# Kernel optimization log

Measured on AMD Instinct MI355X. Metric: run time of the kernel, lower is better.

The kernel has to match this reference:

```python
import jax, jax.numpy as jnp
import numpy as np

B, N, OBS, HID, H = 8, 1024, 64, 192, 3
D = HID // H  # head_dim = 64
ALPHA = 0.2   # LeakyReLU negative slope
NEG = -9e15   # mask value from torch code (-9000000000000000.0)


def gat_layer(h, adj, W, a):
    """Multi-head GAT layer, math-identical to the torch per-head loop.
    h: (B,N,F_in), adj: (N,N), W: (H,F_in,D), a: (H,2D).
    Concat-score a^T [Wh_i || Wh_j] is split into a_l^T Wh_i + a_r^T Wh_j
    (broadcast-add) to avoid materializing the N^2 x 2D tensor.
    """
    Wh = jnp.einsum('bni,hid->bhnd', h, W)           # (B,H,N,D)
    d = Wh.shape[-1]
    s_i = jnp.einsum('bhnd,hd->bhn', Wh, a[:, :d])   # a_l . Wh_i
    s_j = jnp.einsum('bhnd,hd->bhn', Wh, a[:, d:])   # a_r . Wh_j
    e = s_i[..., :, None] + s_j[..., None, :]        # (B,H,N,N)
    e = jnp.where(e > 0, e, ALPHA * e)               # LeakyReLU
    e = jnp.where(adj > 0, e, NEG)                   # adjacency mask
    attn = jax.nn.softmax(e, axis=-1)                # (dropout=0 in eval)
    out = jnp.einsum('bhnm,bhmd->bhnd', attn, Wh)    # weighted aggregate
    b, nh, n, _ = out.shape
    return out.transpose(0, 2, 1, 3).reshape(b, n, nh * d)  # concat heads


def setup_inputs() -> dict:
    key = jax.random.key(0)
    k1, k2, k3, k4, k5 = jax.random.split(key, 5)
    h = jax.random.normal(k1, (B, N, OBS), dtype=jnp.float32)
    adj = jnp.ones((N, N), dtype=jnp.float32)  # graph_type='full'
    # xavier_uniform-style scale (gain=1.414)
    def xav(k, shape, fan_in, fan_out):
        lim = 1.414 * np.sqrt(6.0 / (fan_in + fan_out))
        return jax.random.uniform(k, shape, jnp.float32, -lim, lim)
    W1 = xav(k2, (H, OBS, D), OBS, D)
    a1 = xav(k3, (H, 2 * D), 2 * D, 1)
    W2 = xav(k4, (H, HID, D), HID, D)
    a2 = xav(k5, (H, 2 * D), 2 * D, 1)
    return {"h": h, "adj": adj, "W1": W1, "a1": a1, "W2": W2, "a2": a2}


def reference(h, adj, W1, a1, W2, a2):
    x = gat_layer(h, adj, W1, a1)   # (B,N,HID)
    x = jax.nn.elu(x)               # inter-layer nonlinearity
    x = gat_layer(x, adj, W2, a2)   # (B,N,HID)
    return x
```

## Files before the change

kernel.cpp:

```cpp
#include <hip/hip_runtime.h>
#include <math.h>

#define Bc   8
#define Nc   1024
#define OBSc 64
#define HIDc 192
#define NHc  3
#define Dc   64
#define ALPHAc 0.2f

typedef __attribute__((ext_vector_type(8))) _Float16 half8;
typedef __attribute__((ext_vector_type(4))) float floatx4;


__global__ __launch_bounds__(256) void k_proj1(
    const float* __restrict__ xin, const float* __restrict__ W1,
    const float* __restrict__ a1, _Float16* __restrict__ WhT,
    float* __restrict__ si, float* __restrict__ sj, float* __restrict__ Mp1,
    const float* __restrict__ adj, unsigned long long* __restrict__ adjb,
    const float* __restrict__ W2, _Float16* __restrict__ W2T)
{
    const int tid = threadIdx.x;
    const int bh  = blockIdx.y;

    if (bh == Bc * NHc) {
        const int px = blockIdx.x, wv = tid >> 6, lane = tid & 63;
        for (int r8 = 0; r8 < 8; ++r8) {
            const int i = px * 32 + wv * 8 + r8;
            unsigned long long word = 0;
            for (int g = 0; g < 16; ++g) {
                bool c = adj[(size_t)i * Nc + g * 64 + lane] > 0.f;
                unsigned long long bal = __ballot(c);
                if (lane == g) word = bal;
            }
            if (lane < 16) adjb[(size_t)i * 16 + lane] = word;
        }
        if (px < 12) {
            for (int e = px * 3072 + tid; e < px * 3072 + 3072; e += 256) {
                int t = e & 7, ln = (e >> 3) & 63, p = (e >> 9) & 1, nh = (e >> 10) & 1;
                int g = e >> 11; int ks = g % 6, hh = g / 6;
                int k = ks * 32 + (ln >> 4) * 8 + t;
                int d = nh * 32 + p * 16 + (ln & 15);
                W2T[e] = (_Float16)W2[((size_t)hh * HIDc + k) * Dc + d];
            }
        }
        return;
    }

    __shared__ union {
        _Float16 Bs[64][OBSc + 8];
        _Float16 Ts[64][40];
    } u;
    __shared__ float spsAi[32], spsAj[32], spsBi[32], spsBj[32];

    const int b = bh / NHc, hh = bh % NHc;
    const int row0 = blockIdx.x * 32;

    for (int e = tid; e < OBSc * 64; e += 256) {
        int k = e >> 6, d = e & 63;
        u.Bs[d][k] = (_Float16)W1[(size_t)hh * OBSc * 64 + e];
    }
    __syncthreads();

    const int lane = tid & 63, wv = tid >> 6;
    const int mblk = (wv & 1) * 16, nhalf = (wv >> 1) * 32;
    const int fr = lane & 15, fq = lane >> 4;
    floatx4 acc0 = {0.f,0.f,0.f,0.f}, acc1 = {0.f,0.f,0.f,0.f};
    const int row = row0 + mblk + fr;

#pragma unroll
    for (int ks = 0; ks < OBSc / 32; ++ks) {
        const int k0 = ks * 32 + fq * 8;
        const float* xr = xin + ((size_t)b * Nc + row) * OBSc + k0;
        float4 u0 = *(const float4*)xr;
        float4 u1 = *(const float4*)(xr + 4);
        half8 af;
        af[0] = (_Float16)u0.x; af[1] = (_Float16)u0.y;
        af[2] = (_Float16)u0.z; af[3] = (_Float16)u0.w;
        af[4] = (_Float16)u1.x; af[5] = (_Float16)u1.y;
        af[6] = (_Float16)u1.z; af[7] = (_Float16)u1.w;
        half8 b0 = *(const half8*)&u.Bs[nhalf + fr][k0];
        half8 b1 = *(const half8*)&u.Bs[nhalf + 16 + fr][k0];
        acc0 = __builtin_amdgcn_mfma_f32_16x16x32_f16(af, b0, acc0, 0, 0, 0);
        acc1 = __builtin_amdgcn_mfma_f32_16x16x32_f16(af, b1, acc1, 0, 0, 0);
    }

    const float al0 = a1[hh * 2 * Dc + nhalf + fr];
    const float al1 = a1[hh * 2 * Dc + nhalf + 16 + fr];
    const float ar0 = a1[hh * 2 * Dc + Dc + nhalf + fr];
    const float ar1 = a1[hh * 2 * Dc + Dc + nhalf + 16 + fr];
    float pi[4], pj[4];
#pragma unroll
    for (int r = 0; r < 4; ++r) {
        pi[r] = acc0[r] * al0 + acc1[r] * al1;
        pj[r] = acc0[r] * ar0 + acc1[r] * ar1;
        for (int off = 8; off >= 1; off >>= 1) {
            pi[r] += __shfl_xor(pi[r], off, 64);
            pj[r] += __shfl_xor(pj[r], off, 64);
        }
    }
    if (fr == 0) {
#pragma unroll
        for (int r = 0; r < 4; ++r) {
            int lr = mblk + fq * 4 + r;
            if (nhalf == 0) { spsAi[lr] = pi[r]; spsAj[lr] = pj[r]; }
            else            { spsBi[lr] = pi[r]; spsBj[lr] = pj[r]; }
        }
    }
    __syncthreads();
    if (tid < 64) {
        float vj = -INFINITY;
        if (tid < 32) {
            size_t g = (size_t)bh * Nc + row0 + tid;
            si[g] = spsAi[tid] + spsBi[tid];
            vj    = spsAj[tid] + spsBj[tid];
            sj[g] = vj;
        }
        float mv = vj;
        for (int off = 32; off >= 1; off >>= 1) mv = fmaxf(mv, __shfl_xor(mv, off, 64));
        if (tid == 0) Mp1[bh * 32 + blockIdx.x] = mv;
    }

#pragma unroll
    for (int nt = 0; nt < 2; ++nt) {
        const int d = nhalf + nt * 16 + fr;
        floatx4 acc = nt ? acc1 : acc0;
#pragma unroll
        for (int p = 0; p < 2; ++p) {
            union { unsigned int w; _Float16 h[2]; } pk;
            pk.h[0] = (_Float16)acc[2 * p];
            pk.h[1] = (_Float16)acc[2 * p + 1];
            *(unsigned int*)&u.Ts[d][mblk + fq * 4 + 2 * p] = pk.w;
        }
    }
    __syncthreads();
    {
        const int c2 = tid >> 6, lane2 = tid & 63;
        const int fr2 = lane2 & 15, fq2 = lane2 >> 4;
        const int jt = row0 >> 5;
        uint4 v = *(const uint4*)&u.Ts[c2 * 16 + fr2][fq2 * 8];
        *(uint4*)&WhT[(size_t)(bh * 32 + jt) * 2048 + tid * 8] = v;
    }
}

__global__ __launch_bounds__(384, 2) void k_fused(
    const _Float16* __restrict__ WhT1,
    const float* __restrict__ si1, const float* __restrict__ sj1,
    const float* __restrict__ Mp1, const unsigned long long* __restrict__ adjb,
    const _Float16* __restrict__ W2T, const float* __restrict__ a2,
    _Float16* __restrict__ WhT2,
    float* __restrict__ si2, float* __restrict__ sj2, float* __restrict__ Mp2)
{
    __shared__ union {
        struct { float red[6][64][20]; float zs[6][16]; } ag;
        _Float16 Ts3[3][64][24];
    } uR;
    __shared__ _Float16 xhs[16][208];
    __shared__ float sp2i[6][16], sp2j[6][16];

    const int tid = threadIdx.x, wv = tid >> 6, lane = tid & 63;
    const int b = blockIdx.x >> 6, c16 = blockIdx.x & 63;
    const int row0 = c16 * 16;
    const int hh = wv >> 1, kh = wv & 1;
    const int bh = b * NHc + hh;
    const int fr = lane & 15, fq = lane >> 4;
    const int row = row0 + fr;

    float mpv = Mp1[bh * 32 + (lane & 31)];
    for (int off = 16; off >= 1; off >>= 1) mpv = fmaxf(mpv, __shfl_xor(mpv, off, 64));
    const float s_i = si1[(size_t)bh * Nc + row];
    const float em  = s_i + mpv;
    const float m_i = fmaxf(em, ALPHAc * em);

    const float* sjr = sj1 + (size_t)bh * Nc;
    const unsigned long long* arow = adjb + (size_t)row * 16;
    const _Float16* Bp = WhT1 + (size_t)bh * 65536 + (size_t)kh * 32768 + lane * 8;

    floatx4 acc[4] = {{0.f,0.f,0.f,0.f},{0.f,0.f,0.f,0.f},
                      {0.f,0.f,0.f,0.f},{0.f,0.f,0.f,0.f}};
    float zacc = 0.f;

    float4 sa = *(const float4*)&sjr[(kh * 16) * 32 + fq * 8];
    float4 sb = *(const float4*)&sjr[(kh * 16) * 32 + fq * 8 + 4];
    unsigned long long w = arow[(kh * 16) >> 1];
    half8 bfr0 = *(const half8*)(Bp);
    half8 bfr1 = *(const half8*)(Bp + 512);
    half8 bfr2 = *(const half8*)(Bp + 1024);
    half8 bfr3 = *(const half8*)(Bp + 1536);

#pragma unroll
    for (int s16 = 0; s16 < 16; ++s16) {
        const int s = kh * 16 + s16;
        float4 nsa, nsb; unsigned long long nw;
        half8 nb0, nb1, nb2, nb3;
        if (s16 < 15) {
            const int jn = (s + 1) * 32 + fq * 8;
            nsa = *(const float4*)&sjr[jn];
            nsb = *(const float4*)&sjr[jn + 4];
            nw  = arow[(s + 1) >> 1];
            const _Float16* bn = Bp + (size_t)(s16 + 1) * 2048;
            nb0 = *(const half8*)(bn);
            nb1 = *(const half8*)(bn + 512);
            nb2 = *(const half8*)(bn + 1024);
            nb3 = *(const half8*)(bn + 1536);
        }
        const int bb = (s & 1) * 32 + fq * 8;
        const float sv[8] = {sa.x, sa.y, sa.z, sa.w, sb.x, sb.y, sb.z, sb.w};
        float p[8];
        if (w == ~0ULL) {
#pragma unroll
            for (int t = 0; t < 8; ++t) {
                float e = s_i + sv[t];
                e = fmaxf(e, ALPHAc * e) - m_i;
                p[t] = __expf(e);
            }
        } else {
#pragma unroll
            for (int t = 0; t < 8; ++t) {
                float e = s_i + sv[t];
                e = fmaxf(e, ALPHAc * e) - m_i;
                e = ((w >> (bb + t)) & 1) ? e : -1e30f;
                p[t] = __expf(e);
            }
        }
        zacc += ((p[0] + p[1]) + (p[2] + p[3])) + ((p[4] + p[5]) + (p[6] + p[7]));
        union { half8 v; _Float16 h[8]; } A;
#pragma unroll
        for (int t = 0; t < 8; ++t) A.h[t] = (_Float16)p[t];
        acc[0] = __builtin_amdgcn_mfma_f32_16x16x32_f16(A.v, bfr0, acc[0], 0, 0, 0);
        acc[1] = __builtin_amdgcn_mfma_f32_16x16x32_f16(A.v, bfr1, acc[1], 0, 0, 0);
        acc[2] = __builtin_amdgcn_mfma_f32_16x16x32_f16(A.v, bfr2, acc[2], 0, 0, 0);
        acc[3] = __builtin_amdgcn_mfma_f32_16x16x32_f16(A.v, bfr3, acc[3], 0, 0, 0);
        if (s16 < 15) {
            sa = nsa; sb = nsb; w = nw;
            bfr0 = nb0; bfr1 = nb1; bfr2 = nb2; bfr3 = nb3;
        }
    }

    zacc += __shfl_xor(zacc, 16, 64);
    zacc += __shfl_xor(zacc, 32, 64);
    if (lane < 16) uR.ag.zs[wv][lane] = zacc;
#pragma unroll
    for (int c = 0; c < 4; ++c)
        *(floatx4*)&uR.ag.red[wv][lane][c * 4] = acc[c];
    __syncthreads();

    {
        const int w0 = hh * 2;
#pragma unroll
        for (int cc = 0; cc < 2; ++cc) {
            const int c = kh * 2 + cc;
#pragma unroll
            for (int reg = 0; reg < 4; ++reg) {
                const int r = fq * 4 + reg;
                const float af = uR.ag.red[w0][lane][c * 4 + reg]
                               + uR.ag.red[w0 + 1][lane][c * 4 + reg];
                const float Z = uR.ag.zs[w0][r] + uR.ag.zs[w0 + 1][r];
                float v = af / Z;
                v = v > 0.f ? v : expm1f(v);
                xhs[r][hh * 64 + c * 16 + fr] = (_Float16)v;
            }
        }
    }
    __syncthreads();

    floatx4 a2c0 = {0.f,0.f,0.f,0.f}, a2c1 = {0.f,0.f,0.f,0.f};
#pragma unroll
    for (int ks = 0; ks < 6; ++ks) {
        half8 af2 = *(const half8*)&xhs[fr][ks * 32 + fq * 8];
        const _Float16* wb = W2T + (size_t)((hh * 6 + ks) * 2 + kh) * 1024 + lane * 8;
        half8 b0 = *(const half8*)wb;
        half8 b1 = *(const half8*)(wb + 512);
        a2c0 = __builtin_amdgcn_mfma_f32_16x16x32_f16(af2, b0, a2c0, 0, 0, 0);
        a2c1 = __builtin_amdgcn_mfma_f32_16x16x32_f16(af2, b1, a2c1, 0, 0, 0);
    }

    {
        const float* a2h = a2 + hh * 2 * Dc;
        const float al0 = a2h[kh * 32 + fr];
        const float al1 = a2h[kh * 32 + 16 + fr];
        const float ar0 = a2h[Dc + kh * 32 + fr];
        const float ar1 = a2h[Dc + kh * 32 + 16 + fr];
#pragma unroll
        for (int reg = 0; reg < 4; ++reg) {
            float pi = a2c0[reg] * al0 + a2c1[reg] * al1;
            float pj = a2c0[reg] * ar0 + a2c1[reg] * ar1;
            for (int off = 8; off >= 1; off >>= 1) {
                pi += __shfl_xor(pi, off, 64);
                pj += __shfl_xor(pj, off, 64);
            }
            if (fr == 0) {
                sp2i[wv][fq * 4 + reg] = pi;
                sp2j[wv][fq * 4 + reg] = pj;
            }
        }
    }
    __syncthreads();

    if (kh == 0 && lane < 16) {
        const int r = lane;
        float vi = sp2i[wv][r] + sp2i[wv + 1][r];
        float vj = sp2j[wv][r] + sp2j[wv + 1][r];
        si2[(size_t)bh * Nc + row0 + r] = vi;
        sj2[(size_t)bh * Nc + row0 + r] = vj;
        float mv = vj;
        for (int off = 8; off >= 1; off >>= 1) mv = fmaxf(mv, __shfl_xor(mv, off, 64));
        if (r == 0) Mp2[bh * 64 + c16] = mv;
    }
#pragma unroll
    for (int cc = 0; cc < 2; ++cc) {
        const int d = kh * 32 + cc * 16 + fr;
        floatx4 av = cc ? a2c1 : a2c0;
#pragma unroll
        for (int p = 0; p < 2; ++p) {
            union { unsigned int w2; _Float16 h[2]; } pk;
            pk.h[0] = (_Float16)av[2 * p];
            pk.h[1] = (_Float16)av[2 * p + 1];
            *(unsigned int*)&uR.Ts3[hh][d][fq * 4 + 2 * p] = pk.w2;
        }
    }
    __syncthreads();

    {
        const int hh3 = tid / 128, rem = tid % 128, d3 = rem >> 1, rr = rem & 1;
        uint4 v = *(const uint4*)&uR.Ts3[hh3][d3][rr * 8];
        const int bh3 = b * NHc + hh3;
        const int jt = c16 >> 1;
        const int c3 = d3 >> 4;
        const int fqp = (c16 & 1) * 2 + rr;
        *(uint4*)&WhT2[((((size_t)(bh3 * 32 + jt) * 4 + c3) * 64) + fqp * 16 + (d3 & 15)) * 8] = v;
    }
}

__global__ __launch_bounds__(256, 4) void k_aggr2(
    const _Float16* __restrict__ WhT,
    const float* __restrict__ si, const float* __restrict__ sj,
    const float* __restrict__ Mp2, const unsigned long long* __restrict__ adjb,
    float* __restrict__ out)
{
    __shared__ float red[4][64][20];
    __shared__ float zs[4][16];

    const int tid  = threadIdx.x;
    const int wv   = tid >> 6, lane = tid & 63;
    const int bh   = blockIdx.x >> 6;
    const int row0 = (blockIdx.x & 63) << 4;
    const int b    = bh / NHc, hh = bh % NHc;
    const int fr   = lane & 15, fq = lane >> 4;
    const int row  = row0 + fr;

    float mpv = Mp2[bh * 64 + lane];
    for (int off = 32; off >= 1; off >>= 1) mpv = fmaxf(mpv, __shfl_xor(mpv, off, 64));

    const float s_i = si[(size_t)bh * Nc + row];
    const float em  = s_i + mpv;
    const float m_i = fmaxf(em, ALPHAc * em);

    const float* sjr = sj + (size_t)bh * Nc + fq * 8;
    const unsigned long long* arow = adjb + (size_t)row * 16;
    const _Float16* Bp = WhT + (size_t)bh * 65536 + (size_t)wv * 8 * 2048 + lane * 8;

    floatx4 acc[4] = {{0.f,0.f,0.f,0.f},{0.f,0.f,0.f,0.f},
                      {0.f,0.f,0.f,0.f},{0.f,0.f,0.f,0.f}};
    float zacc = 0.f;

    float4 sa = *(const float4*)&sjr[wv * 256];
    float4 sb = *(const float4*)&sjr[wv * 256 + 4];
    unsigned long long w = arow[(wv * 8) >> 1];
    half8 bfr0 = *(const half8*)(Bp);
    half8 bfr1 = *(const half8*)(Bp + 512);
    half8 bfr2 = *(const half8*)(Bp + 1024);
    half8 bfr3 = *(const half8*)(Bp + 1536);

#pragma unroll
    for (int s8 = 0; s8 < 8; ++s8) {
        const int s = wv * 8 + s8;
        float4 nsa, nsb; unsigned long long nw;
        half8 nb0, nb1, nb2, nb3;
        if (s8 < 7) {
            nsa = *(const float4*)&sjr[(s + 1) * 32];
            nsb = *(const float4*)&sjr[(s + 1) * 32 + 4];
            nw  = arow[(s + 1) >> 1];
            const _Float16* bn = Bp + (size_t)(s8 + 1) * 2048;
            nb0 = *(const half8*)(bn);
            nb1 = *(const half8*)(bn + 512);
            nb2 = *(const half8*)(bn + 1024);
            nb3 = *(const half8*)(bn + 1536);
        }
        const int bb = (s & 1) * 32 + fq * 8;
        const float sv[8] = {sa.x, sa.y, sa.z, sa.w, sb.x, sb.y, sb.z, sb.w};
        float p[8];
        if (w == ~0ULL) {
#pragma unroll
            for (int t = 0; t < 8; ++t) {
                float e = s_i + sv[t];
                e = fmaxf(e, ALPHAc * e) - m_i;
                p[t] = __expf(e);
            }
        } else {
#pragma unroll
            for (int t = 0; t < 8; ++t) {
                float e = s_i + sv[t];
                e = fmaxf(e, ALPHAc * e) - m_i;
                e = ((w >> (bb + t)) & 1) ? e : -1e30f;
                p[t] = __expf(e);
            }
        }
        zacc += ((p[0] + p[1]) + (p[2] + p[3])) + ((p[4] + p[5]) + (p[6] + p[7]));
        union { half8 v; _Float16 h[8]; } A;
#pragma unroll
        for (int t = 0; t < 8; ++t) A.h[t] = (_Float16)p[t];
        acc[0] = __builtin_amdgcn_mfma_f32_16x16x32_f16(A.v, bfr0, acc[0], 0, 0, 0);
        acc[1] = __builtin_amdgcn_mfma_f32_16x16x32_f16(A.v, bfr1, acc[1], 0, 0, 0);
        acc[2] = __builtin_amdgcn_mfma_f32_16x16x32_f16(A.v, bfr2, acc[2], 0, 0, 0);
        acc[3] = __builtin_amdgcn_mfma_f32_16x16x32_f16(A.v, bfr3, acc[3], 0, 0, 0);
        if (s8 < 7) {
            sa = nsa; sb = nsb; w = nw;
            bfr0 = nb0; bfr1 = nb1; bfr2 = nb2; bfr3 = nb3;
        }
    }

    zacc += __shfl_xor(zacc, 16, 64);
    zacc += __shfl_xor(zacc, 32, 64);
    if (lane < 16) zs[wv][lane] = zacc;
#pragma unroll
    for (int c = 0; c < 4; ++c)
        *(floatx4*)&red[wv][lane][c * 4] = acc[c];
    __syncthreads();

    floatx4 af = {0.f, 0.f, 0.f, 0.f};
#pragma unroll
    for (int w2 = 0; w2 < 4; ++w2) {
        floatx4 r = *(const floatx4*)&red[w2][lane][wv * 4];
        af[0] += r[0]; af[1] += r[1]; af[2] += r[2]; af[3] += r[3];
    }
#pragma unroll
    for (int reg = 0; reg < 4; ++reg) {
        const int r = fq * 4 + reg;
        const float Z = (zs[0][r] + zs[1][r]) + (zs[2][r] + zs[3][r]);
        out[((size_t)b * Nc + row0 + r) * HIDc + hh * Dc + wv * 16 + fr] = af[reg] / Z;
    }
}

extern "C" void kernel_launch(void* const* d_in, const int* in_sizes, int n_in,
                              void* d_out, int out_size, void* d_ws, size_t ws_size,
                              hipStream_t stream) {
    const float* h_in = (const float*)d_in[0];
    const float* adj  = (const float*)d_in[1];
    const float* W1   = (const float*)d_in[2];
    const float* a1   = (const float*)d_in[3];
    const float* W2   = (const float*)d_in[4];
    const float* a2   = (const float*)d_in[5];
    float* out = (float*)d_out;

    float* ws = (float*)d_ws;
    const size_t nWhT_f = (size_t)Bc * NHc * Dc * Nc / 2;
    const size_t nAb_f  = (size_t)Nc * 16 * 2;
    const size_t nW2T_f = 36864 / 2;
    const size_t nR     = (size_t)Bc * NHc * Nc;
    _Float16* WhT1 = (_Float16*)ws;
    _Float16* WhT2 = (_Float16*)(ws + nWhT_f);
    unsigned long long* adjb = (unsigned long long*)(ws + 2 * nWhT_f);
    _Float16* W2T  = (_Float16*)(ws + 2 * nWhT_f + nAb_f);
    float* si1 = ws + 2 * nWhT_f + nAb_f + nW2T_f;
    float* sj1 = si1 + nR;
    float* si2 = sj1 + nR;
    float* sj2 = si2 + nR;
    float* Mp1 = sj2 + nR;
    float* Mp2 = Mp1 + 768;

    k_proj1<<<dim3(Nc / 32, Bc * NHc + 1), 256, 0, stream>>>(
        h_in, W1, a1, WhT1, si1, sj1, Mp1, adj, adjb, W2, W2T);

    k_fused<<<512, 384, 0, stream>>>(
        WhT1, si1, sj1, Mp1, adjb, W2T, a2, WhT2, si2, sj2, Mp2);

    k_aggr2<<<1536, 256, 0, stream>>>(WhT2, si2, sj2, Mp2, adjb, out);
}
```

Measured before the change: 119.2 us.

## Stage sj scores and adjacency bits in LDS, deepen WhT prefetch to two stages

Both attention-aggregation kernels now copy the per-head sj score vector and the block's 16 adjacency-bitmask rows into shared memory once, behind a barrier, and read them from LDS inside the main loop instead of issuing global loads per step. The half-precision B-fragment prefetch becomes a three-slot ring buffer loaded two steps ahead instead of one, to hide more global-load latency behind the MFMA work. This costs extra LDS per block (about 14 KB in the fused kernel), more registers for the deeper buffer, and a block-wide sync at the start, any of which may reduce occupancy.

Result: no change. 117.6 us (-1.3%).

```diff
diff --git a/kernel.cpp b/kernel.cpp
--- a/kernel.cpp
+++ b/kernel.cpp
@@ -157,6 +157,8 @@
     } uR;
     __shared__ _Float16 xhs[16][208];
     __shared__ float sp2i[6][16], sp2j[6][16];
+    __shared__ float sjs[3][1024];
+    __shared__ unsigned long long adjs[16][16];
 
     const int tid = threadIdx.x, wv = tid >> 6, lane = tid & 63;
     const int b = blockIdx.x >> 6, c16 = blockIdx.x & 63;
@@ -166,44 +168,47 @@
     const int fr = lane & 15, fq = lane >> 4;
     const int row = row0 + fr;
 
+    for (int e = tid; e < 768; e += 384) {
+        int h = e >> 8, idx = (e & 255) * 4;
+        *(float4*)&sjs[h][idx] = *(const float4*)&sj1[(size_t)(b * NHc + h) * Nc + idx];
+    }
+    if (tid < 256)
+        adjs[tid >> 4][tid & 15] = adjb[(size_t)(row0 + (tid >> 4)) * 16 + (tid & 15)];
+    __syncthreads();
+
     float mpv = Mp1[bh * 32 + (lane & 31)];
     for (int off = 16; off >= 1; off >>= 1) mpv = fmaxf(mpv, __shfl_xor(mpv, off, 64));
     const float s_i = si1[(size_t)bh * Nc + row];
     const float em  = s_i + mpv;
     const float m_i = fmaxf(em, ALPHAc * em);
 
-    const float* sjr = sj1 + (size_t)bh * Nc;
-    const unsigned long long* arow = adjb + (size_t)row * 16;
     const _Float16* Bp = WhT1 + (size_t)bh * 65536 + (size_t)kh * 32768 + lane * 8;
 
     floatx4 acc[4] = {{0.f,0.f,0.f,0.f},{0.f,0.f,0.f,0.f},
                       {0.f,0.f,0.f,0.f},{0.f,0.f,0.f,0.f}};
     float zacc = 0.f;
 
-    float4 sa = *(const float4*)&sjr[(kh * 16) * 32 + fq * 8];
-    float4 sb = *(const float4*)&sjr[(kh * 16) * 32 + fq * 8 + 4];
-    unsigned long long w = arow[(kh * 16) >> 1];
-    half8 bfr0 = *(const half8*)(Bp);
-    half8 bfr1 = *(const half8*)(Bp + 512);
-    half8 bfr2 = *(const half8*)(Bp + 1024);
-    half8 bfr3 = *(const half8*)(Bp + 1536);
+    half8 bf[3][4];
+#pragma unroll
+    for (int st = 0; st < 2; ++st)
+#pragma unroll
+        for (int c = 0; c < 4; ++c)
+            bf[st][c] = *(const half8*)(Bp + (size_t)st * 2048 + c * 512);
 
 #pragma unroll
     for (int s16 = 0; s16 < 16; ++s16) {
-        const int s = kh * 16 + s16;
-        float4 nsa, nsb; unsigned long long nw;
-        half8 nb0, nb1, nb2, nb3;
-        if (s16 < 15) {
-            const int jn = (s + 1) * 32 + fq * 8;
-            nsa = *(const float4*)&sjr[jn];
-            nsb = *(const float4*)&sjr[jn + 4];
-            nw  = arow[(s + 1) >> 1];
-            const _Float16* bn = Bp + (size_t)(s16 + 1) * 2048;
-            nb0 = *(const half8*)(bn);
-            nb1 = *(const half8*)(bn + 512);
-            nb2 = *(const half8*)(bn + 1024);
-            nb3 = *(const half8*)(bn + 1536);
-        }
+        const int s   = kh * 16 + s16;
+        const int cur = s16 % 3;
+        if (s16 < 14) {
+            const int nxt = (s16 + 2) % 3;
+            const _Float16* bn = Bp + (size_t)(s16 + 2) * 2048;
+#pragma unroll
+            for (int c = 0; c < 4; ++c)
+                bf[nxt][c] = *(const half8*)(bn + c * 512);
+        }
+        const float4 sa = *(const float4*)&sjs[hh][s * 32 + fq * 8];
+        const float4 sb = *(const float4*)&sjs[hh][s * 32 + fq * 8 + 4];
+        const unsigned long long w = adjs[fr][s >> 1];
         const int bb = (s & 1) * 32 + fq * 8;
         const float sv[8] = {sa.x, sa.y, sa.z, sa.w, sb.x, sb.y, sb.z, sb.w};
         float p[8];
@@ -227,14 +232,10 @@
         union { half8 v; _Float16 h[8]; } A;
 #pragma unroll
         for (int t = 0; t < 8; ++t) A.h[t] = (_Float16)p[t];
-        acc[0] = __builtin_amdgcn_mfma_f32_16x16x32_f16(A.v, bfr0, acc[0], 0, 0, 0);
-        acc[1] = __builtin_amdgcn_mfma_f32_16x16x32_f16(A.v, bfr1, acc[1], 0, 0, 0);
-        acc[2] = __builtin_amdgcn_mfma_f32_16x16x32_f16(A.v, bfr2, acc[2], 0, 0, 0);
-        acc[3] = __builtin_amdgcn_mfma_f32_16x16x32_f16(A.v, bfr3, acc[3], 0, 0, 0);
-        if (s16 < 15) {
-            sa = nsa; sb = nsb; w = nw;
-            bfr0 = nb0; bfr1 = nb1; bfr2 = nb2; bfr3 = nb3;
-        }
+        acc[0] = __builtin_amdgcn_mfma_f32_16x16x32_f16(A.v, bf[cur][0], acc[0], 0, 0, 0);
+        acc[1] = __builtin_amdgcn_mfma_f32_16x16x32_f16(A.v, bf[cur][1], acc[1], 0, 0, 0);
+        acc[2] = __builtin_amdgcn_mfma_f32_16x16x32_f16(A.v, bf[cur][2], acc[2], 0, 0, 0);
+        acc[3] = __builtin_amdgcn_mfma_f32_16x16x32_f16(A.v, bf[cur][3], acc[3], 0, 0, 0);
     }
 
     zacc += __shfl_xor(zacc, 16, 64);
@@ -340,6 +341,8 @@
 {
     __shared__ float red[4][64][20];
     __shared__ float zs[4][16];
+    __shared__ float sjs[1024];
+    __shared__ unsigned long long adjs[16][16];
 
     const int tid  = threadIdx.x;
     const int wv   = tid >> 6, lane = tid & 63;
@@ -349,6 +352,13 @@
     const int fr   = lane & 15, fq = lane >> 4;
     const int row  = row0 + fr;
 
+    for (int e = tid; e < 256; e += 256)
+        *(float4*)&sjs[e * 4] = *(const float4*)&sj[(size_t)bh * Nc + e * 4];
+    if (tid < 256 && tid >= 0) {  }
+    if (tid < 256)
+        adjs[tid >> 4][tid & 15] = adjb[(size_t)(row0 + (tid >> 4)) * 16 + (tid & 15)];
+    __syncthreads();
+
     float mpv = Mp2[bh * 64 + lane];
     for (int off = 32; off >= 1; off >>= 1) mpv = fmaxf(mpv, __shfl_xor(mpv, off, 64));
 
@@ -356,37 +366,33 @@
     const float em  = s_i + mpv;
     const float m_i = fmaxf(em, ALPHAc * em);
 
-    const float* sjr = sj + (size_t)bh * Nc + fq * 8;
-    const unsigned long long* arow = adjb + (size_t)row * 16;
     const _Float16* Bp = WhT + (size_t)bh * 65536 + (size_t)wv * 8 * 2048 + lane * 8;
 
     floatx4 acc[4] = {{0.f,0.f,0.f,0.f},{0.f,0.f,0.f,0.f},
                       {0.f,0.f,0.f,0.f},{0.f,0.f,0.f,0.f}};
     float zacc = 0.f;
 
-    float4 sa = *(const float4*)&sjr[wv * 256];
-    float4 sb = *(const float4*)&sjr[wv * 256 + 4];
-    unsigned long long w = arow[(wv * 8) >> 1];
-    half8 bfr0 = *(const half8*)(Bp);
-    half8 bfr1 = *(const half8*)(Bp + 512);
-    half8 bfr2 = *(const half8*)(Bp + 1024);
-    half8 bfr3 = *(const half8*)(Bp + 1536);
+    half8 bf[3][4];
+#pragma unroll
+    for (int st = 0; st < 2; ++st)
+#pragma unroll
+        for (int c = 0; c < 4; ++c)
+            bf[st][c] = *(const half8*)(Bp + (size_t)st * 2048 + c * 512);
 
 #pragma unroll
     for (int s8 = 0; s8 < 8; ++s8) {
-        const int s = wv * 8 + s8;
-        float4 nsa, nsb; unsigned long long nw;
-        half8 nb0, nb1, nb2, nb3;
-        if (s8 < 7) {
-            nsa = *(const float4*)&sjr[(s + 1) * 32];
-            nsb = *(const float4*)&sjr[(s + 1) * 32 + 4];
-            nw  = arow[(s + 1) >> 1];
-            const _Float16* bn = Bp + (size_t)(s8 + 1) * 2048;
-            nb0 = *(const half8*)(bn);
-            nb1 = *(const half8*)(bn + 512);
-            nb2 = *(const half8*)(bn + 1024);
-            nb3 = *(const half8*)(bn + 1536);
-        }
+        const int s   = wv * 8 + s8;
+        const int cur = s8 % 3;
+        if (s8 < 6) {
+            const int nxt = (s8 + 2) % 3;
+            const _Float16* bn = Bp + (size_t)(s8 + 2) * 2048;
+#pragma unroll
+            for (int c = 0; c < 4; ++c)
+                bf[nxt][c] = *(const half8*)(bn + c * 512);
+        }
+        const float4 sa = *(const float4*)&sjs[s * 32 + fq * 8];
+        const float4 sb = *(const float4*)&sjs[s * 32 + fq * 8 + 4];
+        const unsigned long long w = adjs[fr][s >> 1];
         const int bb = (s & 1) * 32 + fq * 8;
         const float sv[8] = {sa.x, sa.y, sa.z, sa.w, sb.x, sb.y, sb.z, sb.w};
         float p[8];
@@ -410,14 +416,10 @@
         union { half8 v; _Float16 h[8]; } A;
 #pragma unroll
         for (int t = 0; t < 8; ++t) A.h[t] = (_Float16)p[t];
-        acc[0] = __builtin_amdgcn_mfma_f32_16x16x32_f16(A.v, bfr0, acc[0], 0, 0, 0);
-        acc[1] = __builtin_amdgcn_mfma_f32_16x16x32_f16(A.v, bfr1, acc[1], 0, 0, 0);
-        acc[2] = __builtin_amdgcn_mfma_f32_16x16x32_f16(A.v, bfr2, acc[2], 0, 0, 0);
-        acc[3] = __builtin_amdgcn_mfma_f32_16x16x32_f16(A.v, bfr3, acc[3], 0, 0, 0);
-        if (s8 < 7) {
-            sa = nsa; sb = nsb; w = nw;
-            bfr0 = nb0; bfr1 = nb1; bfr2 = nb2; bfr3 = nb3;
-        }
+        acc[0] = __builtin_amdgcn_mfma_f32_16x16x32_f16(A.v, bf[cur][0], acc[0], 0, 0, 0);
+        acc[1] = __builtin_amdgcn_mfma_f32_16x16x32_f16(A.v, bf[cur][1], acc[1], 0, 0, 0);
+        acc[2] = __builtin_amdgcn_mfma_f32_16x16x32_f16(A.v, bf[cur][2], acc[2], 0, 0, 0);
+        acc[3] = __builtin_amdgcn_mfma_f32_16x16x32_f16(A.v, bf[cur][3], acc[3], 0, 0, 0);
     }
 
     zacc += __shfl_xor(zacc, 16, 64);
```
